# Kernel tuning notes

Hardware: AMD Instinct MI355X
Metric: run time of the kernel (lower is better)

Reference implementation:

```python
import jax, jax.numpy as jnp
import numpy as np

INPUT_SIZE = 256
HIDDEN_SIZE = 256


def setup_inputs() -> dict:
    key = jax.random.key(0)
    k_x, k_wxh, k_whh = jax.random.split(key, 3)
    x = jax.random.normal(k_x, (64, 2048, INPUT_SIZE), dtype=jnp.float32)
    # torch nn.Linear weights: [out_features, in_features]
    W_xh = jax.random.normal(k_wxh, (HIDDEN_SIZE, INPUT_SIZE), dtype=jnp.float32) / np.sqrt(INPUT_SIZE)
    W_hh = jax.random.normal(k_whh, (HIDDEN_SIZE, HIDDEN_SIZE), dtype=jnp.float32) / np.sqrt(HIDDEN_SIZE)
    b_h = jnp.zeros((HIDDEN_SIZE,), dtype=jnp.float32)
    return {"x": x, "W_xh": W_xh, "W_hh": W_hh, "b_h": b_h}


def reference(x, W_xh, W_hh, b_h):
    # x: [B, T, D]; h_t = relu(x_t @ W_xh^T + h_{t-1} @ W_hh^T + b_h)
    B, T, _ = x.shape
    # Precompute input projection for all timesteps in one GEMM (same math).
    xproj = jnp.einsum('btd,hd->bth', x, W_xh) + b_h  # [B, T, H]

    def step(h, xp_t):
        h_new = jax.nn.relu(xp_t + h @ W_hh.T)
        return h_new, h_new

    h0 = jnp.zeros((B, HIDDEN_SIZE), dtype=x.dtype)
    # scan over time axis: move T to leading dim
    _, hs = jax.lax.scan(step, h0, jnp.swapaxes(xproj, 0, 1))  # hs: [T, B, H]
    return jnp.swapaxes(hs, 0, 1)  # [B, T, H]
```

## Files before the change

### kernel.cpp

```cpp
#include <hip/hip_runtime.h>

#define BATCH 64
#define SEQT  2048
#define DIM   256
#define HID   256

typedef _Float16 half_t;
typedef _Float16 half2_t __attribute__((ext_vector_type(2)));
typedef _Float16 half4_t __attribute__((ext_vector_type(4)));
typedef _Float16 half8_t __attribute__((ext_vector_type(8)));
typedef float    float4_t __attribute__((ext_vector_type(4)));

__device__ __forceinline__ half8_t cvt8(float4_t a, float4_t b) {
  half8_t r;
  r[0] = (half_t)a[0]; r[1] = (half_t)a[1]; r[2] = (half_t)a[2]; r[3] = (half_t)a[3];
  r[4] = (half_t)b[0]; r[5] = (half_t)b[1]; r[6] = (half_t)b[2]; r[7] = (half_t)b[3];
  return r;
}
#define H2X(v, c) __builtin_shufflevector((v), (v), 2*(c), 2*(c)+1)

template<int CTRL>
__device__ __forceinline__ float dpp_mov(float a) {
  int t = __builtin_amdgcn_mov_dpp(__builtin_bit_cast(int, a), CTRL, 0xF, 0xF, true);
  return __builtin_bit_cast(float, t);
}

__global__ __launch_bounds__(256) void cvt_w_kernel(
    const float* __restrict__ W, half_t* __restrict__ Wh)
{
  const int i = (blockIdx.x * 256 + threadIdx.x) * 4;
  float4_t v = *(const float4_t*)(W + i);
  half4_t o; o[0]=(half_t)v[0]; o[1]=(half_t)v[1]; o[2]=(half_t)v[2]; o[3]=(half_t)v[3];
  *(half4_t*)(Wh + i) = o;
}

__global__ __launch_bounds__(256) void xproj_f16_kernel(
    const float* __restrict__ x, const half_t* __restrict__ Wh,
    const float* __restrict__ bh, float* __restrict__ out)
{
  const int lane = threadIdx.x & 63;
  const int wave = threadIdx.x >> 6;
  const int r16  = lane & 15;
  const int kg   = lane >> 4;
  const long m0  = (long)blockIdx.x * 64 + wave * 16;

  half8_t a[8];
  const float* xr = x + (m0 + r16) * (long)DIM + kg * 8;
  #pragma unroll
  for (int kf = 0; kf < 8; ++kf) {
    float4_t x0 = *(const float4_t*)(xr + kf * 32);
    float4_t x1 = *(const float4_t*)(xr + kf * 32 + 4);
    a[kf] = cvt8(x0, x1);
  }

  #pragma unroll 2
  for (int nt = 0; nt < 16; ++nt) {
    const half_t* wr = Wh + (nt * 16 + r16) * (long)DIM + kg * 8;
    float bb = bh[nt * 16 + r16];
    float4_t acc = {bb, bb, bb, bb};
    #pragma unroll
    for (int kf = 0; kf < 8; ++kf) {
      half8_t bfrag = *(const half8_t*)(wr + kf * 32);
      acc = __builtin_amdgcn_mfma_f32_16x16x32_f16(a[kf], bfrag, acc, 0, 0, 0);
    }
    float* op = out + (m0 + kg * 4) * (long)HID + nt * 16 + r16;
    #pragma unroll
    for (int r = 0; r < 4; ++r) op[(long)r * HID] = acc[r];
  }
}

__global__ __launch_bounds__(256) void xproj_kernel(
    const float* __restrict__ x, const float* __restrict__ Wxh,
    const float* __restrict__ bh, float* __restrict__ out)
{
  const int lane = threadIdx.x & 63;
  const int wave = threadIdx.x >> 6;
  const int r16  = lane & 15;
  const int kg   = lane >> 4;
  const long m0  = (long)blockIdx.x * 64 + wave * 16;

  half8_t a[8];
  const float* xr = x + (m0 + r16) * (long)DIM + kg * 8;
  #pragma unroll
  for (int kf = 0; kf < 8; ++kf) {
    float4_t x0 = *(const float4_t*)(xr + kf * 32);
    float4_t x1 = *(const float4_t*)(xr + kf * 32 + 4);
    a[kf] = cvt8(x0, x1);
  }
  for (int nt = 0; nt < 16; ++nt) {
    const float* wr = Wxh + (nt * 16 + r16) * (long)DIM + kg * 8;
    float bb = bh[nt * 16 + r16];
    float4_t acc = {bb, bb, bb, bb};
    #pragma unroll
    for (int kf = 0; kf < 8; ++kf) {
      float4_t w0 = *(const float4_t*)(wr + kf * 32);
      float4_t w1 = *(const float4_t*)(wr + kf * 32 + 4);
      acc = __builtin_amdgcn_mfma_f32_16x16x32_f16(a[kf], cvt8(w0, w1), acc, 0, 0, 0);
    }
    float* op = out + (m0 + kg * 4) * (long)HID + nt * 16 + r16;
    #pragma unroll
    for (int r = 0; r < 4; ++r) op[(long)r * HID] = acc[r];
  }
}

#define RNN_BAR() asm volatile("s_waitcnt lgkmcnt(0)\n\ts_barrier" ::: "memory")

#define RNN_STEP(U, XQ)                                                        \
  {                                                                            \
    const int t = t4 + (U);                                                    \
         \
    const int tp = (t + 4 < T) ? (t + 4) : (T - 1);                            \
    float xnew = outp[(long)tp * HID];                                         \
    half8_t hv[4];                                                             \
    _Pragma("unroll")                                                          \
    for (int s = 0; s < 4; ++s)                                                \
      hv[s] = *(const half8_t*)(hraw[(U) & 1] + rb + 16 * s);                  \
    float a0 = 0.f, a1 = 0.f, a2 = 0.f, a3 = 0.f;                              \
    _Pragma("unroll")                                                          \
    for (int s = 0; s < 4; ++s) {                                              \
      a0 = __builtin_amdgcn_fdot2(H2X(w8[0][s], 0), H2X(hv[s], 0), a0, false); \
      a0 = __builtin_amdgcn_fdot2(H2X(w8[0][s], 1), H2X(hv[s], 1), a0, false); \
      a0 = __builtin_amdgcn_fdot2(H2X(w8[0][s], 2), H2X(hv[s], 2), a0, false); \
      a0 = __builtin_amdgcn_fdot2(H2X(w8[0][s], 3), H2X(hv[s], 3), a0, false); \
      a1 = __builtin_amdgcn_fdot2(H2X(w8[1][s], 0), H2X(hv[s], 0), a1, false); \
      a1 = __builtin_amdgcn_fdot2(H2X(w8[1][s], 1), H2X(hv[s], 1), a1, false); \
      a1 = __builtin_amdgcn_fdot2(H2X(w8[1][s], 2), H2X(hv[s], 2), a1, false); \
      a1 = __builtin_amdgcn_fdot2(H2X(w8[1][s], 3), H2X(hv[s], 3), a1, false); \
      a2 = __builtin_amdgcn_fdot2(H2X(w8[2][s], 0), H2X(hv[s], 0), a2, false); \
      a2 = __builtin_amdgcn_fdot2(H2X(w8[2][s], 1), H2X(hv[s], 1), a2, false); \
      a2 = __builtin_amdgcn_fdot2(H2X(w8[2][s], 2), H2X(hv[s], 2), a2, false); \
      a2 = __builtin_amdgcn_fdot2(H2X(w8[2][s], 3), H2X(hv[s], 3), a2, false); \
      a3 = __builtin_amdgcn_fdot2(H2X(w8[3][s], 0), H2X(hv[s], 0), a3, false); \
      a3 = __builtin_amdgcn_fdot2(H2X(w8[3][s], 1), H2X(hv[s], 1), a3, false); \
      a3 = __builtin_amdgcn_fdot2(H2X(w8[3][s], 2), H2X(hv[s], 2), a3, false); \
      a3 = __builtin_amdgcn_fdot2(H2X(w8[3][s], 3), H2X(hv[s], 3), a3, false); \
    }                                                                          \
        \
    float r0 = kA ? a0 : a2;                 \
    float r1 = kA ? a1 : a3;                                                   \
    float b0 = (kA ? a2 : a0) + dpp_mov<0x141>(r0);                            \
    float b1 = (kA ? a3 : a1) + dpp_mov<0x141>(r1);                            \
    float rB = kB ? b0 : b1;                 \
    float c  = (kB ? b1 : b0) + dpp_mov<0x4E>(rB);                             \
    float fin = c + dpp_mov<0xB1>(c);            \
    float y = fmaxf(fin + (XQ), 0.f);                                          \
    outp[(long)t * HID] = y;                                                   \
    *(half_t*)(hraw[((U) & 1) ^ 1] + hwb) = (half_t)y;                         \
    XQ = xnew;                                                                 \
    RNN_BAR();                                                                 \
  }

__global__ __launch_bounds__(512, 1) void rnn_kernel(
    const float* __restrict__ Whh, float* __restrict__ out, int T)
{
  __shared__ alignas(128) unsigned char hraw[2][8 * 80];

  const int tid = threadIdx.x;
  const int l   = tid & 63;
  const int w   = tid >> 6;
  const int g   = l & 7;
  const int j0  = w * 32 + (l >> 3) * 4;
  const int rb  = g * 80;
  const int jown = j0 + ((l >> 1) & 3);
  const int hwb = ((jown >> 5) * 80 + (jown & 31) * 2);
  const bool kA = (l & 4) != 0;
  const bool kB = (l & 2) != 0;
  float* outp = out + (long)blockIdx.x * SEQT * HID + jown;

  half8_t w8[4][4];
  #pragma unroll
  for (int i = 0; i < 4; ++i) {
    const float* wr = Whh + (long)(j0 + i) * HID + g * 32;
    #pragma unroll
    for (int s = 0; s < 4; ++s) {
      float4_t v0 = *(const float4_t*)(wr + s * 8);
      float4_t v1 = *(const float4_t*)(wr + s * 8 + 4);
      w8[i][s] = cvt8(v0, v1);
    }
  }

  if (tid < 160) ((float*)hraw[0])[tid] = 0.f;

  float xq0 = outp[0L * HID];
  float xq1 = outp[1L * HID];
  float xq2 = outp[2L * HID];
  float xq3 = outp[3L * HID];
  RNN_BAR();

  #pragma unroll 1
  for (int t4 = 0; t4 < T; t4 += 4) {
    RNN_STEP(0, xq0)
    RNN_STEP(1, xq1)
    RNN_STEP(2, xq2)
    RNN_STEP(3, xq3)
  }
}

extern "C" void kernel_launch(void* const* d_in, const int* in_sizes, int n_in,
                              void* d_out, int out_size, void* d_ws, size_t ws_size,
                              hipStream_t stream) {
  const float* x   = (const float*)d_in[0];
  const float* Wxh = (const float*)d_in[1];
  const float* Whh = (const float*)d_in[2];
  const float* bh  = (const float*)d_in[3];
  float* out = (float*)d_out;

  if (ws_size >= (size_t)(DIM * HID * sizeof(half_t))) {
    half_t* Wh = (half_t*)d_ws;
    cvt_w_kernel<<<dim3((DIM * HID) / 1024), dim3(256), 0, stream>>>(Wxh, Wh);
    xproj_f16_kernel<<<dim3((BATCH * SEQT) / 64), dim3(256), 0, stream>>>(x, Wh, bh, out);
  } else {
    xproj_kernel<<<dim3((BATCH * SEQT) / 64), dim3(256), 0, stream>>>(x, Wxh, bh, out);
  }
  rnn_kernel<<<dim3(BATCH), dim3(512), 0, stream>>>(Whh, out, SEQT);
}
```

Baseline: 989.7 us.

## Accumulate recurrence in packed fp16 FMA and keep W_xh fragments in registers

The recurrent step now uses packed half2 FMAs with fp16 accumulators instead of fdot2 into fp32, converting to float only at the end. This is meant to shorten the serial per-step dependency chain. The input-projection GEMM is restructured so each wave holds its W fragments in registers and loops over 8 row tiles, cutting repeated weight loads. The fp16 accumulation over 64 terms per lane risks lower accuracy.

```diff
diff --git a/kernel.cpp b/kernel.cpp
--- a/kernel.cpp
+++ b/kernel.cpp
@@ -19,12 +19,22 @@
 }
 #define H2X(v, c) __builtin_shufflevector((v), (v), 2*(c), 2*(c)+1)
 
+__device__ __forceinline__ half2_t pkfma(half2_t a, half2_t b, half2_t c) {
+#if __has_builtin(__builtin_elementwise_fma)
+  return __builtin_elementwise_fma(a, b, c);
+#else
+  return a * b + c;
+#endif
+}
+
 template<int CTRL>
 __device__ __forceinline__ float dpp_mov(float a) {
   int t = __builtin_amdgcn_mov_dpp(__builtin_bit_cast(int, a), CTRL, 0xF, 0xF, true);
   return __builtin_bit_cast(float, t);
 }
 
+#define RNN_BAR() asm volatile("s_waitcnt lgkmcnt(0)\n\ts_barrier" ::: "memory")
+
 __global__ __launch_bounds__(256) void cvt_w_kernel(
     const float* __restrict__ W, half_t* __restrict__ Wh)
 {
@@ -34,8 +44,53 @@
   *(half4_t*)(Wh + i) = o;
 }
 
-__global__ __launch_bounds__(256) void xproj_f16_kernel(
+__global__ __launch_bounds__(256) void xproj_f16_v2(
     const float* __restrict__ x, const half_t* __restrict__ Wh,
+    const float* __restrict__ bh, float* __restrict__ out)
+{
+  const int lane = threadIdx.x & 63;
+  const int wave = threadIdx.x >> 6;
+  const int r16  = lane & 15;
+  const int kg   = lane >> 4;
+  const long m0  = (long)blockIdx.x * 128;
+
+  half8_t bfr[4][8];
+  float bb[4];
+  #pragma unroll
+  for (int qq = 0; qq < 4; ++qq) {
+    const int nt = wave * 4 + qq;
+    const half_t* wr = Wh + (nt * 16 + r16) * (long)DIM + kg * 8;
+    #pragma unroll
+    for (int kf = 0; kf < 8; ++kf)
+      bfr[qq][kf] = *(const half8_t*)(wr + kf * 32);
+    bb[qq] = bh[nt * 16 + r16];
+  }
+  #pragma unroll 1
+  for (int mi = 0; mi < 8; ++mi) {
+    const long mrow = m0 + mi * 16;
+    half8_t a[8];
+    const float* xr = x + (mrow + r16) * (long)DIM + kg * 8;
+    #pragma unroll
+    for (int kf = 0; kf < 8; ++kf) {
+      float4_t x0 = *(const float4_t*)(xr + kf * 32);
+      float4_t x1 = *(const float4_t*)(xr + kf * 32 + 4);
+      a[kf] = cvt8(x0, x1);
+    }
+    #pragma unroll
+    for (int qq = 0; qq < 4; ++qq) {
+      float4_t acc = {bb[qq], bb[qq], bb[qq], bb[qq]};
+      #pragma unroll
+      for (int kf = 0; kf < 8; ++kf)
+        acc = __builtin_amdgcn_mfma_f32_16x16x32_f16(a[kf], bfr[qq][kf], acc, 0, 0, 0);
+      float* op = out + (mrow + kg * 4) * (long)HID + (wave * 4 + qq) * 16 + r16;
+      #pragma unroll
+      for (int r = 0; r < 4; ++r) op[(long)r * HID] = acc[r];
+    }
+  }
+}
+
+__global__ __launch_bounds__(256) void xproj_kernel(
+    const float* __restrict__ x, const float* __restrict__ Wxh,
     const float* __restrict__ bh, float* __restrict__ out)
 {
   const int lane = threadIdx.x & 63;
@@ -52,41 +107,6 @@
     float4_t x1 = *(const float4_t*)(xr + kf * 32 + 4);
     a[kf] = cvt8(x0, x1);
   }
-
-  #pragma unroll 2
-  for (int nt = 0; nt < 16; ++nt) {
-    const half_t* wr = Wh + (nt * 16 + r16) * (long)DIM + kg * 8;
-    float bb = bh[nt * 16 + r16];
-    float4_t acc = {bb, bb, bb, bb};
-    #pragma unroll
-    for (int kf = 0; kf < 8; ++kf) {
-      half8_t bfrag = *(const half8_t*)(wr + kf * 32);
-      acc = __builtin_amdgcn_mfma_f32_16x16x32_f16(a[kf], bfrag, acc, 0, 0, 0);
-    }
-    float* op = out + (m0 + kg * 4) * (long)HID + nt * 16 + r16;
-    #pragma unroll
-    for (int r = 0; r < 4; ++r) op[(long)r * HID] = acc[r];
-  }
-}
-
-__global__ __launch_bounds__(256) void xproj_kernel(
-    const float* __restrict__ x, const float* __restrict__ Wxh,
-    const float* __restrict__ bh, float* __restrict__ out)
-{
-  const int lane = threadIdx.x & 63;
-  const int wave = threadIdx.x >> 6;
-  const int r16  = lane & 15;
-  const int kg   = lane >> 4;
-  const long m0  = (long)blockIdx.x * 64 + wave * 16;
-
-  half8_t a[8];
-  const float* xr = x + (m0 + r16) * (long)DIM + kg * 8;
-  #pragma unroll
-  for (int kf = 0; kf < 8; ++kf) {
-    float4_t x0 = *(const float4_t*)(xr + kf * 32);
-    float4_t x1 = *(const float4_t*)(xr + kf * 32 + 4);
-    a[kf] = cvt8(x0, x1);
-  }
   for (int nt = 0; nt < 16; ++nt) {
     const float* wr = Wxh + (nt * 16 + r16) * (long)DIM + kg * 8;
     float bb = bh[nt * 16 + r16];
@@ -103,38 +123,39 @@
   }
 }
 
-#define RNN_BAR() asm volatile("s_waitcnt lgkmcnt(0)\n\ts_barrier" ::: "memory")
-
 #define RNN_STEP(U, XQ)                                                        \
   {                                                                            \
     const int t = t4 + (U);                                                    \
-         \
     const int tp = (t + 4 < T) ? (t + 4) : (T - 1);                            \
     float xnew = outp[(long)tp * HID];                                         \
     half8_t hv[4];                                                             \
     _Pragma("unroll")                                                          \
     for (int s = 0; s < 4; ++s)                                                \
       hv[s] = *(const half8_t*)(hraw[(U) & 1] + rb + 16 * s);                  \
-    float a0 = 0.f, a1 = 0.f, a2 = 0.f, a3 = 0.f;                              \
+    half2_t p0 = {0, 0}, p1 = {0, 0}, p2 = {0, 0}, p3 = {0, 0};                \
     _Pragma("unroll")                                                          \
     for (int s = 0; s < 4; ++s) {                                              \
-      a0 = __builtin_amdgcn_fdot2(H2X(w8[0][s], 0), H2X(hv[s], 0), a0, false); \
-      a0 = __builtin_amdgcn_fdot2(H2X(w8[0][s], 1), H2X(hv[s], 1), a0, false); \
-      a0 = __builtin_amdgcn_fdot2(H2X(w8[0][s], 2), H2X(hv[s], 2), a0, false); \
-      a0 = __builtin_amdgcn_fdot2(H2X(w8[0][s], 3), H2X(hv[s], 3), a0, false); \
-      a1 = __builtin_amdgcn_fdot2(H2X(w8[1][s], 0), H2X(hv[s], 0), a1, false); \
-      a1 = __builtin_amdgcn_fdot2(H2X(w8[1][s], 1), H2X(hv[s], 1), a1, false); \
-      a1 = __builtin_amdgcn_fdot2(H2X(w8[1][s], 2), H2X(hv[s], 2), a1, false); \
-      a1 = __builtin_amdgcn_fdot2(H2X(w8[1][s], 3), H2X(hv[s], 3), a1, false); \
-      a2 = __builtin_amdgcn_fdot2(H2X(w8[2][s], 0), H2X(hv[s], 0), a2, false); \
-      a2 = __builtin_amdgcn_fdot2(H2X(w8[2][s], 1), H2X(hv[s], 1), a2, false); \
-      a2 = __builtin_amdgcn_fdot2(H2X(w8[2][s], 2), H2X(hv[s], 2), a2, false); \
-      a2 = __builtin_amdgcn_fdot2(H2X(w8[2][s], 3), H2X(hv[s], 3), a2, false); \
-      a3 = __builtin_amdgcn_fdot2(H2X(w8[3][s], 0), H2X(hv[s], 0), a3, false); \
-      a3 = __builtin_amdgcn_fdot2(H2X(w8[3][s], 1), H2X(hv[s], 1), a3, false); \
-      a3 = __builtin_amdgcn_fdot2(H2X(w8[3][s], 2), H2X(hv[s], 2), a3, false); \
-      a3 = __builtin_amdgcn_fdot2(H2X(w8[3][s], 3), H2X(hv[s], 3), a3, false); \
+      p0 = pkfma(H2X(w8[0][s], 0), H2X(hv[s], 0), p0);                         \
+      p0 = pkfma(H2X(w8[0][s], 1), H2X(hv[s], 1), p0);                         \
+      p0 = pkfma(H2X(w8[0][s], 2), H2X(hv[s], 2), p0);                         \
+      p0 = pkfma(H2X(w8[0][s], 3), H2X(hv[s], 3), p0);                         \
+      p1 = pkfma(H2X(w8[1][s], 0), H2X(hv[s], 0), p1);                         \
+      p1 = pkfma(H2X(w8[1][s], 1), H2X(hv[s], 1), p1);                         \
+      p1 = pkfma(H2X(w8[1][s], 2), H2X(hv[s], 2), p1);                         \
+      p1 = pkfma(H2X(w8[1][s], 3), H2X(hv[s], 3), p1);                         \
+      p2 = pkfma(H2X(w8[2][s], 0), H2X(hv[s], 0), p2);                         \
+      p2 = pkfma(H2X(w8[2][s], 1), H2X(hv[s], 1), p2);                         \
+      p2 = pkfma(H2X(w8[2][s], 2), H2X(hv[s], 2), p2);                         \
+      p2 = pkfma(H2X(w8[2][s], 3), H2X(hv[s], 3), p2);                         \
+      p3 = pkfma(H2X(w8[3][s], 0), H2X(hv[s], 0), p3);                         \
+      p3 = pkfma(H2X(w8[3][s], 1), H2X(hv[s], 1), p3);                         \
+      p3 = pkfma(H2X(w8[3][s], 2), H2X(hv[s], 2), p3);                         \
+      p3 = pkfma(H2X(w8[3][s], 3), H2X(hv[s], 3), p3);                         \
     }                                                                          \
+    float a0 = (float)p0[0] + (float)p0[1];                                    \
+    float a1 = (float)p1[0] + (float)p1[1];                                    \
+    float a2 = (float)p2[0] + (float)p2[1];                                    \
+    float a3 = (float)p3[0] + (float)p3[1];                                    \
         \
     float r0 = kA ? a0 : a2;                 \
     float r1 = kA ? a1 : a3;                                                   \
@@ -208,7 +229,7 @@
   if (ws_size >= (size_t)(DIM * HID * sizeof(half_t))) {
     half_t* Wh = (half_t*)d_ws;
     cvt_w_kernel<<<dim3((DIM * HID) / 1024), dim3(256), 0, stream>>>(Wxh, Wh);
-    xproj_f16_kernel<<<dim3((BATCH * SEQT) / 64), dim3(256), 0, stream>>>(x, Wh, bh, out);
+    xproj_f16_v2<<<dim3((BATCH * SEQT) / 128), dim3(256), 0, stream>>>(x, Wh, bh, out);
   } else {
     xproj_kernel<<<dim3((BATCH * SEQT) / 64), dim3(256), 0, stream>>>(x, Wxh, bh, out);
   }
```

Result: slower. 1.019 ms (+3.0%).
